# Kernel optimization log

Measured on AMD Instinct MI355X. Metric: run time of the kernel, lower is better.

## Reference

```python
import jax, jax.numpy as jnp
import numpy as np

N = 100000      # nodes
E = 1600000     # directed edges (before self-loops)
IN = 128        # in_channels
HID = 64        # hidden_channels
LH = 4          # local heads
GH = 2          # global heads
NC = 2          # num_classes
BN_EPS = 1e-5
NEG_SLOPE = 0.2


def setup_inputs() -> dict:
    key = jax.random.key(0)
    ks = jax.random.split(key, 24)
    def nrm(k, shape, fan_in):
        return jax.random.normal(k, shape, dtype=jnp.float32) / np.sqrt(fan_in)
    inp = {
        "x": jax.random.normal(ks[0], (N, IN), dtype=jnp.float32),
        "edge_index": jax.random.randint(ks[1], (2, E), 0, N, dtype=jnp.int64),
        # local GATConv: IN -> HID, heads=LH, concat
        "w1": nrm(ks[2], (IN, LH * HID), IN),
        "a_src1": nrm(ks[3], (LH, HID), HID),
        "a_dst1": nrm(ks[4], (LH, HID), HID),
        "b1": jnp.zeros((LH * HID,), jnp.float32),
        # BN1 over LH*HID
        "g1": jnp.ones((LH * HID,), jnp.float32),
        "be1": jnp.zeros((LH * HID,), jnp.float32),
        "m1": 0.1 * jax.random.normal(ks[5], (LH * HID,), dtype=jnp.float32),
        "v1": 0.5 + jax.random.uniform(ks[6], (LH * HID,), dtype=jnp.float32),
        # global GATConv: LH*HID -> HID, heads=GH, concat=False (mean)
        "w2": nrm(ks[7], (LH * HID, GH * HID), LH * HID),
        "a_src2": nrm(ks[8], (GH, HID), HID),
        "a_dst2": nrm(ks[9], (GH, HID), HID),
        "b2": jnp.zeros((HID,), jnp.float32),
        # BN2 over HID
        "g2": jnp.ones((HID,), jnp.float32),
        "be2": jnp.zeros((HID,), jnp.float32),
        "m2": 0.1 * jax.random.normal(ks[10], (HID,), dtype=jnp.float32),
        "v2": 0.5 + jax.random.uniform(ks[11], (HID,), dtype=jnp.float32),
        # classifier HID -> NC
        "wc": nrm(ks[12], (HID, NC), HID),
        "bc": jnp.zeros((NC,), jnp.float32),
    }
    return inp


def _gat_conv(x, src, dst, W, att_src, att_dst, bias, heads, out_c, concat):
    n = x.shape[0]
    h = (x @ W).reshape(n, heads, out_c)           # [N,H,C]
    a_s = jnp.sum(h * att_src, axis=-1)            # [N,H]
    a_d = jnp.sum(h * att_dst, axis=-1)            # [N,H]
    e = jax.nn.leaky_relu(a_s[src] + a_d[dst], NEG_SLOPE)  # [E,H]
    # segment softmax over destination node
    mx = jax.ops.segment_max(e, dst, num_segments=n)
    e = jnp.exp(e - mx[dst])
    den = jax.ops.segment_sum(e, dst, num_segments=n)
    alpha = e / (den[dst] + 1e-16)                 # [E,H]
    msg = h[src] * alpha[:, :, None]               # [E,H,C]
    out = jax.ops.segment_sum(msg, dst, num_segments=n)   # [N,H,C]
    out = out.reshape(n, heads * out_c) if concat else out.mean(axis=1)
    return out + bias


def _bn_eval(x, gamma, beta, mean, var):
    return (x - mean) * (gamma / jnp.sqrt(var + BN_EPS)) + beta


def reference(x, edge_index, w1, a_src1, a_dst1, b1, g1, be1, m1, v1,
              w2, a_src2, a_dst2, b2, g2, be2, m2, v2, wc, bc):
    n = x.shape[0]
    loops = jnp.arange(n, dtype=edge_index.dtype)
    src = jnp.concatenate([edge_index[0], loops])  # PyG adds self-loops
    dst = jnp.concatenate([edge_index[1], loops])
    # local attention layer
    h = _gat_conv(x, src, dst, w1, a_src1, a_dst1, b1, LH, HID, True)
    h = jax.nn.elu(_bn_eval(h, g1, be1, m1, v1))
    # global attention layer (last: mean over heads, no activation)
    h = _gat_conv(h, src, dst, w2, a_src2, a_dst2, b2, GH, HID, False)
    h = _bn_eval(h, g2, be2, m2, v2)
    return h @ wc + bc                             # [N, NC] logits
```

## Files before the change

kernel.cpp:

```cpp
#include <hip/hip_runtime.h>
#include <hip/hip_fp16.h>
#include <math.h>

#define NN 100000
#define EE 1600000
#define ETOT (EE + NN)
#define BN_EPS 1e-5f
#define NEG_SLOPE 0.2f
#define NBLK ((NN + 255) / 256)
#define GXM ((NN + 127) / 128)
#define NGRP 8
#define GRPSZ ((NN + NGRP - 1) / NGRP)

typedef _Float16 half8 __attribute__((ext_vector_type(8)));
typedef float f32x4 __attribute__((ext_vector_type(4)));

__device__ __forceinline__ float lrelu(float x) { return fmaxf(x, NEG_SLOPE * x); }
__device__ __forceinline__ float wsum(float v) {
#pragma unroll
    for (int m = 32; m; m >>= 1) v += __shfl_xor(v, m, 64);
    return v;
}
__device__ __forceinline__ float gsum16(float v) {
#pragma unroll
    for (int m = 1; m < 16; m <<= 1) v += __shfl_xor(v, m, 64);
    return v;
}
__device__ __forceinline__ unsigned packh2(float a, float b) {
    __half2 p = __float22half2_rn(make_float2(a, b));
    return *reinterpret_cast<unsigned*>(&p);
}

__global__ __launch_bounds__(256) void k_hist8(const int* __restrict__ ei,
                                               int* __restrict__ counts) {
    const int g = blockIdx.x & (NGRP - 1);
    const int lo = g * GRPSZ;
    const int hi = (lo + GRPSZ < NN) ? lo + GRPSZ : NN;
    const int nb = gridDim.x >> 3;
    const int stride = nb * 256;
    for (int e = (blockIdx.x >> 3) * 256 + threadIdx.x; e < EE; e += stride) {
        const int d = ei[EE + e];
        if (d >= lo && d < hi) atomicAdd(&counts[d], 1);
    }
}
__global__ __launch_bounds__(256) void k_scatter8(const int* __restrict__ ei,
                                                  int* __restrict__ srcs,
                                                  int* __restrict__ cursor) {
    const int g = blockIdx.x & (NGRP - 1);
    const int lo = g * GRPSZ;
    const int hi = (lo + GRPSZ < NN) ? lo + GRPSZ : NN;
    const int nb = gridDim.x >> 3;
    const int stride = nb * 256;
    for (int e = (blockIdx.x >> 3) * 256 + threadIdx.x; e < EE; e += stride) {
        const int d = ei[EE + e];
        if (d >= lo && d < hi) {
            const int p = atomicAdd(&cursor[d], 1);
            srcs[p] = ei[e];
        }
    }
}
__global__ __launch_bounds__(256) void k_scan_bsum(const int* __restrict__ counts,
                                                   int* __restrict__ bsum) {
    __shared__ int sd[256];
    const int i = blockIdx.x * 256 + threadIdx.x;
    sd[threadIdx.x] = (i < NN) ? counts[i] + 1 : 0;
    __syncthreads();
    for (int s2 = 128; s2; s2 >>= 1) {
        if (threadIdx.x < s2) sd[threadIdx.x] += sd[threadIdx.x + s2];
        __syncthreads();
    }
    if (threadIdx.x == 0) bsum[blockIdx.x] = sd[0];
}
__global__ __launch_bounds__(512) void k_scan_top(int* __restrict__ bsum, int nb) {
    __shared__ int sd[512];
    const int t = threadIdx.x;
    const int orig = (t < nb) ? bsum[t] : 0;
    sd[t] = orig;
    __syncthreads();
    for (int off = 1; off < 512; off <<= 1) {
        const int v = (t >= off) ? sd[t - off] : 0;
        __syncthreads();
        sd[t] += v;
        __syncthreads();
    }
    if (t < nb) bsum[t] = sd[t] - orig;
}
__global__ __launch_bounds__(256) void k_scan_final(const int* __restrict__ counts,
                                                    const int* __restrict__ bsum_ex,
                                                    int* __restrict__ rowptr,
                                                    int* __restrict__ srcs,
                                                    int* __restrict__ cursor) {
    __shared__ int sd[256];
    const int i = blockIdx.x * 256 + threadIdx.x;
    const int orig = (i < NN) ? counts[i] + 1 : 0;
    sd[threadIdx.x] = orig;
    __syncthreads();
    for (int off = 1; off < 256; off <<= 1) {
        const int v = (threadIdx.x >= off) ? sd[threadIdx.x - off] : 0;
        __syncthreads();
        sd[threadIdx.x] += v;
        __syncthreads();
    }
    if (i < NN) {
        const int rp = bsum_ex[blockIdx.x] + sd[threadIdx.x] - orig;
        rowptr[i] = rp;
        srcs[rp] = i;
        cursor[i] = rp + 1;
        if (i == NN - 1) rowptr[NN] = ETOT;
    }
}

__global__ __launch_bounds__(256) void k_prep(
    const float* __restrict__ b1, const float* __restrict__ g1,
    const float* __restrict__ be1, const float* __restrict__ m1,
    const float* __restrict__ v1,
    const float* __restrict__ b2, const float* __restrict__ g2,
    const float* __restrict__ be2, const float* __restrict__ m2,
    const float* __restrict__ v2, const float* __restrict__ wc,
    const float* __restrict__ bc,
    const float* __restrict__ w1, const float* __restrict__ w2,
    const float* __restrict__ as1w, const float* __restrict__ ad1w,
    float* __restrict__ scs, float* __restrict__ shs,
    float* __restrict__ wq, float* __restrict__ cst,
    float* __restrict__ va, float* __restrict__ vd,
    _Float16* __restrict__ wt1, _Float16* __restrict__ wt2,
    int* __restrict__ counts)
{
    const int b = blockIdx.x, t = threadIdx.x;
    if (b == 0) {
        const float sc = g1[t] * rsqrtf(v1[t] + BN_EPS);
        scs[t] = sc;
        shs[t] = (b1[t] - m1[t]) * sc + be1[t];
    } else if (b == 1) {
        if (t < 64) {
            const float s2 = g2[t] * rsqrtf(v2[t] + BN_EPS);
            wq[t * 2 + 0] = s2 * wc[t * 2 + 0];
            wq[t * 2 + 1] = s2 * wc[t * 2 + 1];
            const float tv = (b2[t] - m2[t]) * s2 + be2[t];
            const float c0 = wsum(tv * wc[t * 2 + 0]);
            const float c1 = wsum(tv * wc[t * 2 + 1]);
            if (t == 0) { cst[0] = c0 + bc[0]; cst[1] = c1 + bc[1]; }
        }
    } else if (b < 130) {
        const int idx = (b - 2) * 256 + t;
        const int n = idx >> 7, k = idx & 127;
        wt1[idx] = (_Float16)w1[k * 256 + n];
    } else if (b < 258) {
        const int idx = (b - 130) * 256 + t;
        const int n = idx >> 8, k = idx & 255;
        wt2[idx] = (_Float16)w2[k * 128 + n];
    } else if (b == 258) {
#pragma unroll
        for (int rep = 0; rep < 2; ++rep) {
            const int idx = rep * 256 + t;
            const int h = idx >> 7, k = idx & 127;
            float sa = 0.f, sd = 0.f;
            for (int c = 0; c < 64; ++c) {
                const float wv = w1[k * 256 + h * 64 + c];
                sa = fmaf(wv, as1w[h * 64 + c], sa);
                sd = fmaf(wv, ad1w[h * 64 + c], sd);
            }
            va[idx] = sa;
            vd[idx] = sd;
        }
    } else {
        const int i = (b - 259) * 256 + t;
        if (i < NN) counts[i] = 0;
    }
}

__global__ __launch_bounds__(256) void k_xcvt(
    const float* __restrict__ x, const float* __restrict__ va,
    const float* __restrict__ vd, _Float16* __restrict__ xh,
    float* __restrict__ as_, float* __restrict__ ad_)
{
    const int gid = blockIdx.x * 256 + threadIdx.x;
    const int n = gid >> 4;
    if (n >= NN) return;
    const int j = gid & 15;
    const int k0 = j * 8;
    float xv[8];
    *(float4*)&xv[0] = *(const float4*)&x[(size_t)n * 128 + k0];
    *(float4*)&xv[4] = *(const float4*)&x[(size_t)n * 128 + k0 + 4];
    half8 hv;
#pragma unroll
    for (int i = 0; i < 8; ++i) hv[i] = (_Float16)xv[i];
    *(half8*)&xh[(size_t)n * 128 + k0] = hv;
    float sa[4], sd[4];
#pragma unroll
    for (int h = 0; h < 4; ++h) {
        float s = 0.f, d = 0.f;
#pragma unroll
        for (int i = 0; i < 8; ++i) {
            s = fmaf(xv[i], va[h * 128 + k0 + i], s);
            d = fmaf(xv[i], vd[h * 128 + k0 + i], d);
        }
        sa[h] = gsum16(s);
        sd[h] = gsum16(d);
    }
    if (j == 0) {
        *(float4*)&as_[n * 4] = make_float4(sa[0], sa[1], sa[2], sa[3]);
        *(float4*)&ad_[n * 4] = make_float4(sd[0], sd[1], sd[2], sd[3]);
    }
}

__global__ __launch_bounds__(256) void k_agg1x(
    const int* __restrict__ rowptr, const int* __restrict__ srcs,
    const _Float16* __restrict__ xh, const float* __restrict__ as_,
    const float* __restrict__ ad_, _Float16* __restrict__ y)
{
    const int d = blockIdx.x * 4 + (threadIdx.x >> 6);
    if (d >= NN) return;
    const int lane = threadIdx.x & 63;
    const int r0 = rowptr[d], r1 = rowptr[d + 1];
    const int h = lane >> 4;
    const int cb = (lane & 15) * 8;
    const float myad = ad_[d * 4 + h];

    float den = 0.f;
    float acc[8] = {0.f, 0.f, 0.f, 0.f, 0.f, 0.f, 0.f, 0.f};
    int k = r0;
    for (; k + 3 < r1; k += 4) {
        const int s0 = srcs[k], s1 = srcs[k + 1], s2 = srcs[k + 2], s3 = srcs[k + 3];
        const float p0 = __expf(lrelu(as_[s0 * 4 + h] + myad));
        const float p1 = __expf(lrelu(as_[s1 * 4 + h] + myad));
        const float p2 = __expf(lrelu(as_[s2 * 4 + h] + myad));
        const float p3 = __expf(lrelu(as_[s3 * 4 + h] + myad));
        const half8 v0 = *(const half8*)&xh[(size_t)s0 * 128 + cb];
        const half8 v1 = *(const half8*)&xh[(size_t)s1 * 128 + cb];
        const half8 v2 = *(const half8*)&xh[(size_t)s2 * 128 + cb];
        const half8 v3 = *(const half8*)&xh[(size_t)s3 * 128 + cb];
        den += (p0 + p1) + (p2 + p3);
#pragma unroll
        for (int i = 0; i < 8; ++i) {
            acc[i] = fmaf(p0, (float)v0[i], acc[i]);
            acc[i] = fmaf(p1, (float)v1[i], acc[i]);
            acc[i] = fmaf(p2, (float)v2[i], acc[i]);
            acc[i] = fmaf(p3, (float)v3[i], acc[i]);
        }
    }
    for (; k < r1; ++k) {
        const int s = srcs[k];
        const float p = __expf(lrelu(as_[s * 4 + h] + myad));
        den += p;
        const half8 v = *(const half8*)&xh[(size_t)s * 128 + cb];
#pragma unroll
        for (int i = 0; i < 8; ++i) acc[i] = fmaf(p, (float)v[i], acc[i]);
    }
    const float inv = 1.f / (den + 1e-16f);
    half8 hv;
#pragma unroll
    for (int i = 0; i < 8; ++i) hv[i] = (_Float16)(acc[i] * inv);
    *(half8*)&y[(size_t)d * 512 + h * 128 + cb] = hv;
}

__global__ __launch_bounds__(256) void k_bd1(
    const _Float16* __restrict__ y, const _Float16* __restrict__ wt,
    const float* __restrict__ scs, const float* __restrict__ shs,
    _Float16* __restrict__ agg)
{
    __shared__ _Float16 ys[128][136];
    const int n0 = blockIdx.x * 128;
    const int t = threadIdx.x;
    const int l = t & 63, w = t >> 6;
    const int m0w = (w & 1) * 64, n0w = (w >> 1) * 32;
    const int lc = l & 15, kq = (l >> 4) * 8, lr = (l >> 4) * 4;

    for (int h = 0; h < 4; ++h) {
        if (h) __syncthreads();
#pragma unroll
        for (int i = 0; i < 8; ++i) {
            const int f = i * 2048 + t * 8;
            const int m = f >> 7, k8 = f & 127;
            half8 v = {};
            if (n0 + m < NN)
                v = *(const half8*)&y[(size_t)(n0 + m) * 512 + h * 128 + k8];
            *(half8*)&ys[m][k8] = v;
        }
        __syncthreads();

        const f32x4 fzero = {0.f, 0.f, 0.f, 0.f};
        f32x4 acc[4][2];
#pragma unroll
        for (int r = 0; r < 4; ++r) { acc[r][0] = fzero; acc[r][1] = fzero; }

#pragma unroll
        for (int ks = 0; ks < 4; ++ks) {
            const int k0 = ks * 32 + kq;
            const half8 a0 = *(const half8*)&ys[m0w + 0  + lc][k0];
            const half8 a1 = *(const half8*)&ys[m0w + 16 + lc][k0];
            const half8 a2 = *(const half8*)&ys[m0w + 32 + lc][k0];
            const half8 a3 = *(const half8*)&ys[m0w + 48 + lc][k0];
#pragma unroll
            for (int c = 0; c < 2; ++c) {
                const half8 b = *(const half8*)&wt[(size_t)(h * 64 + n0w + c * 16 + lc) * 128 + k0];
                acc[0][c] = __builtin_amdgcn_mfma_f32_16x16x32_f16(a0, b, acc[0][c], 0, 0, 0);
                acc[1][c] = __builtin_amdgcn_mfma_f32_16x16x32_f16(a1, b, acc[1][c], 0, 0, 0);
                acc[2][c] = __builtin_amdgcn_mfma_f32_16x16x32_f16(a2, b, acc[2][c], 0, 0, 0);
                acc[3][c] = __builtin_amdgcn_mfma_f32_16x16x32_f16(a3, b, acc[3][c], 0, 0, 0);
            }
        }

        const int j0 = h * 64 + n0w + lc;
        const float sc0 = scs[j0],      sh0 = shs[j0];
        const float sc1 = scs[j0 + 16], sh1 = shs[j0 + 16];
#pragma unroll
        for (int r = 0; r < 4; ++r) {
#pragma unroll
            for (int i = 0; i < 4; ++i) {
                const int rg = n0 + m0w + r * 16 + lr + i;
                if (rg < NN) {
                    float e0 = fmaf(acc[r][0][i], sc0, sh0);
                    float e1 = fmaf(acc[r][1][i], sc1, sh1);
                    e0 = e0 > 0.f ? e0 : __expf(e0) - 1.f;
                    e1 = e1 > 0.f ? e1 : __expf(e1) - 1.f;
                    _Float16* ap = agg + (size_t)rg * 256 + j0;
                    ap[0]  = (_Float16)e0;
                    ap[16] = (_Float16)e1;
                }
            }
        }
    }
}

__global__ __launch_bounds__(256) void k_gemm2m(
    const _Float16* __restrict__ agg, const _Float16* __restrict__ wt,
    const float* __restrict__ asrc, const float* __restrict__ adst,
    const float* __restrict__ wq,
    float* __restrict__ ad_, uint2* __restrict__ pack)
{
    __shared__ _Float16 xs[128][136];
    const int n0 = blockIdx.x * 128;
    const int t = threadIdx.x;
    const int l = t & 63, w = t >> 6;
    const int m0w = (w & 1) * 64, n0w = (w >> 1) * 64;
    const int lc = l & 15, kq = (l >> 4) * 8, lr = (l >> 4) * 4;

    const f32x4 fzero = {0.f, 0.f, 0.f, 0.f};
    f32x4 acc[4][4];
#pragma unroll
    for (int r = 0; r < 4; ++r)
#pragma unroll
        for (int c = 0; c < 4; ++c) acc[r][c] = fzero;

    const _Float16* abase = agg + (size_t)n0 * 256;
    for (int kc = 0; kc < 2; ++kc) {
        if (kc) __syncthreads();
#pragma unroll
        for (int i = 0; i < 8; ++i) {
            const int f = i * 2048 + t * 8;
            const int m = f >> 7, k8 = f & 127;
            half8 v = {};
            if (n0 + m < NN)
                v = *(const half8*)(abase + (size_t)m * 256 + kc * 128 + k8);
            *(half8*)&xs[m][k8] = v;
        }
        __syncthreads();

#pragma unroll
        for (int ks = 0; ks < 4; ++ks) {
            const int k0 = ks * 32 + kq;
            const int kgf = kc * 128 + k0;
            const half8 a0 = *(const half8*)&xs[m0w + 0  + lc][k0];
            const half8 a1 = *(const half8*)&xs[m0w + 16 + lc][k0];
            const half8 a2 = *(const half8*)&xs[m0w + 32 + lc][k0];
            const half8 a3 = *(const half8*)&xs[m0w + 48 + lc][k0];
#pragma unroll
            for (int c = 0; c < 4; ++c) {
                const half8 b = *(const half8*)&wt[(size_t)(n0w + c * 16 + lc) * 256 + kgf];
                acc[0][c] = __builtin_amdgcn_mfma_f32_16x16x32_f16(a0, b, acc[0][c], 0, 0, 0);
                acc[1][c] = __builtin_amdgcn_mfma_f32_16x16x32_f16(a1, b, acc[1][c], 0, 0, 0);
                acc[2][c] = __builtin_amdgcn_mfma_f32_16x16x32_f16(a2, b, acc[2][c], 0, 0, 0);
                acc[3][c] = __builtin_amdgcn_mfma_f32_16x16x32_f16(a3, b, acc[3][c], 0, 0, 0);
            }
        }
    }

    const int head = n0w >> 6;
    float awv[4], dwv[4], wq0[4], wq1[4];
#pragma unroll
    for (int c = 0; c < 4; ++c) {
        const int j = n0w + c * 16 + lc;
        const int cl = j & 63;
        awv[c] = asrc[j];
        dwv[c] = adst[j];
        wq0[c] = wq[cl * 2 + 0];
        wq1[c] = wq[cl * 2 + 1];
    }
#pragma unroll
    for (int r = 0; r < 4; ++r) {
#pragma unroll
        for (int i = 0; i < 4; ++i) {
            float s = 0.f, d = 0.f, q0 = 0.f, q1 = 0.f;
#pragma unroll
            for (int c = 0; c < 4; ++c) {
                s = fmaf(acc[r][c][i], awv[c], s);
                d = fmaf(acc[r][c][i], dwv[c], d);
                q0 = fmaf(acc[r][c][i], wq0[c], q0);
                q1 = fmaf(acc[r][c][i], wq1[c], q1);
            }
            s = gsum16(s); d = gsum16(d); q0 = gsum16(q0); q1 = gsum16(q1);
            const int rg = n0 + m0w + r * 16 + lr + i;
            if (lc == 0 && rg < NN) {
                ad_[rg * 2 + head] = d;
                uint2 u;
                u.x = __float_as_uint(s);
                u.y = packh2(q0, q1);
                pack[rg * 2 + head] = u;
            }
        }
    }
}

__global__ __launch_bounds__(256) void k_agg2q(
    const int* __restrict__ rowptr, const int* __restrict__ srcs,
    const uint4* __restrict__ pack, const float* __restrict__ ad_,
    const float* __restrict__ cst, float* __restrict__ out)
{
    const int d = blockIdx.x * 16 + (threadIdx.x >> 4);
    if (d >= NN) return;
    const int il = threadIdx.x & 15;
    const int r0 = rowptr[d], r1 = rowptr[d + 1];
    const float2 adv = *(const float2*)&ad_[d * 2];

    float den0 = 0.f, den1 = 0.f;
    float qa00 = 0.f, qa01 = 0.f, qa10 = 0.f, qa11 = 0.f;
    for (int k = r0 + il; k < r1; k += 16) {
        const int s = srcs[k];
        const uint4 rec = pack[s];
        const float a0 = __uint_as_float(rec.x);
        const float a1 = __uint_as_float(rec.z);
        const float2 q0 = __half22float2(*reinterpret_cast<const __half2*>(&rec.y));
        const float2 q1 = __half22float2(*reinterpret_cast<const __half2*>(&rec.w));
        const float p0 = __expf(lrelu(a0 + adv.x));
        const float p1 = __expf(lrelu(a1 + adv.y));
        den0 += p0; den1 += p1;
        qa00 = fmaf(p0, q0.x, qa00); qa01 = fmaf(p0, q0.y, qa01);
        qa10 = fmaf(p1, q1.x, qa10); qa11 = fmaf(p1, q1.y, qa11);
    }
    den0 = gsum16(den0); den1 = gsum16(den1);
    qa00 = gsum16(qa00); qa01 = gsum16(qa01);
    qa10 = gsum16(qa10); qa11 = gsum16(qa11);
    if (il == 0) {
        const float i0 = 1.f / (den0 + 1e-16f);
        const float i1 = 1.f / (den1 + 1e-16f);
        out[d * 2 + 0] = cst[0] + 0.5f * (qa00 * i0 + qa10 * i1);
        out[d * 2 + 1] = cst[1] + 0.5f * (qa01 * i0 + qa11 * i1);
    }
}

extern "C" void kernel_launch(void* const* d_in, const int* in_sizes, int n_in,
                              void* d_out, int out_size, void* d_ws, size_t ws_size,
                              hipStream_t stream) {
    const float* x      = (const float*)d_in[0];
    const int*   ei     = (const int*)d_in[1];
    const float* w1     = (const float*)d_in[2];
    const float* a_src1 = (const float*)d_in[3];
    const float* a_dst1 = (const float*)d_in[4];
    const float* b1     = (const float*)d_in[5];
    const float* g1     = (const float*)d_in[6];
    const float* be1    = (const float*)d_in[7];
    const float* m1     = (const float*)d_in[8];
    const float* v1     = (const float*)d_in[9];
    const float* w2     = (const float*)d_in[10];
    const float* a_src2 = (const float*)d_in[11];
    const float* a_dst2 = (const float*)d_in[12];
    const float* b2     = (const float*)d_in[13];
    const float* g2     = (const float*)d_in[14];
    const float* be2    = (const float*)d_in[15];
    const float* m2     = (const float*)d_in[16];
    const float* v2     = (const float*)d_in[17];
    const float* wc     = (const float*)d_in[18];
    const float* bc     = (const float*)d_in[19];
    float* out = (float*)d_out;

    float* ws = (float*)d_ws;
    _Float16* xh    = (_Float16*)ws;
    _Float16* y     = (_Float16*)(ws + (size_t)NN * 64);
    _Float16* agg1h = (_Float16*)(ws + (size_t)NN * 320);
    float* C = ws + (size_t)NN * 448;

    float* as1 = C;
    float* ad1 = C + (size_t)NN * 4;
    float* ad2 = C + (size_t)NN * 8;
    float* packf = C + (size_t)NN * 10;
    float* scs = C + (size_t)NN * 14;
    float* shs = scs + 256;
    float* wq  = shs + 256;
    float* cst = wq + 128;
    float* va  = cst + 64;
    float* vd  = va + 512;
    float* wbase = vd + 512;
    _Float16* wt1 = (_Float16*)wbase;
    _Float16* wt2 = wt1 + 32768;
    int* counts = (int*)(wbase + 32768);
    int* rowptr = counts + NN;
    int* bsum   = rowptr + NN + 63;
    int* srcs   = bsum + 512;

    k_prep<<<259 + NBLK, 256, 0, stream>>>(b1, g1, be1, m1, v1, b2, g2, be2, m2, v2,
                                           wc, bc, w1, w2, a_src1, a_dst1,
                                           scs, shs, wq, cst, va, vd, wt1, wt2, counts);
    k_hist8<<<2048, 256, 0, stream>>>(ei, counts);
    k_scan_bsum<<<NBLK, 256, 0, stream>>>(counts, bsum);
    k_scan_top<<<1, 512, 0, stream>>>(bsum, NBLK);
    k_scan_final<<<NBLK, 256, 0, stream>>>(counts, bsum, rowptr, srcs, counts);
    k_scatter8<<<2048, 256, 0, stream>>>(ei, srcs, counts);

    k_xcvt<<<(NN * 16 + 255) / 256, 256, 0, stream>>>(x, va, vd, xh, as1, ad1);
    k_agg1x<<<(NN + 3) / 4, 256, 0, stream>>>(rowptr, srcs, xh, as1, ad1, y);
    k_bd1<<<GXM, 256, 0, stream>>>(y, wt1, scs, shs, agg1h);

    k_gemm2m<<<GXM, 256, 0, stream>>>(agg1h, wt2, a_src2, a_dst2, wq,
                                      ad2, (uint2*)packf);
    k_agg2q<<<(NN + 15) / 16, 256, 0, stream>>>(rowptr, srcs, (const uint4*)packf,
                                                ad2, cst, out);
}
```

Measured before the change: 378.0 us.

## Fuse layer-1 GEMM with layer-2 GEMM, merge hist into prep, collapse scan kernels

Fuses the per-head layer-1 projection+BN+ELU GEMM with the layer-2 GEMM through a shared-memory intermediate, so the 256-wide fp16 activation never round-trips through global memory. The degree histogram is folded into the prep kernel, with counts zeroed by a memset. The top-level scan is merged into the final scan by having each block reduce the preceding block sums. The agg1 loop now loads srcs/attention scores once per lane and broadcasts them with shuffles. Tiles shrink to 64 rows with more shared memory per block, and the redundant block-sum reads in every scan block add some work.

New measurement: 360.2 us. -4.7%, faster.

```diff
diff --git a/kernel.cpp b/kernel.cpp
--- a/kernel.cpp
+++ b/kernel.cpp
@@ -8,9 +8,9 @@
 #define BN_EPS 1e-5f
 #define NEG_SLOPE 0.2f
 #define NBLK ((NN + 255) / 256)
-#define GXM ((NN + 127) / 128)
 #define NGRP 8
 #define GRPSZ ((NN + NGRP - 1) / NGRP)
+#define HISTBLK 2048
 
 typedef _Float16 half8 __attribute__((ext_vector_type(8)));
 typedef float f32x4 __attribute__((ext_vector_type(4)));
@@ -31,86 +31,7 @@
     return *reinterpret_cast<unsigned*>(&p);
 }
 
-__global__ __launch_bounds__(256) void k_hist8(const int* __restrict__ ei,
-                                               int* __restrict__ counts) {
-    const int g = blockIdx.x & (NGRP - 1);
-    const int lo = g * GRPSZ;
-    const int hi = (lo + GRPSZ < NN) ? lo + GRPSZ : NN;
-    const int nb = gridDim.x >> 3;
-    const int stride = nb * 256;
-    for (int e = (blockIdx.x >> 3) * 256 + threadIdx.x; e < EE; e += stride) {
-        const int d = ei[EE + e];
-        if (d >= lo && d < hi) atomicAdd(&counts[d], 1);
-    }
-}
-__global__ __launch_bounds__(256) void k_scatter8(const int* __restrict__ ei,
-                                                  int* __restrict__ srcs,
-                                                  int* __restrict__ cursor) {
-    const int g = blockIdx.x & (NGRP - 1);
-    const int lo = g * GRPSZ;
-    const int hi = (lo + GRPSZ < NN) ? lo + GRPSZ : NN;
-    const int nb = gridDim.x >> 3;
-    const int stride = nb * 256;
-    for (int e = (blockIdx.x >> 3) * 256 + threadIdx.x; e < EE; e += stride) {
-        const int d = ei[EE + e];
-        if (d >= lo && d < hi) {
-            const int p = atomicAdd(&cursor[d], 1);
-            srcs[p] = ei[e];
-        }
-    }
-}
-__global__ __launch_bounds__(256) void k_scan_bsum(const int* __restrict__ counts,
-                                                   int* __restrict__ bsum) {
-    __shared__ int sd[256];
-    const int i = blockIdx.x * 256 + threadIdx.x;
-    sd[threadIdx.x] = (i < NN) ? counts[i] + 1 : 0;
-    __syncthreads();
-    for (int s2 = 128; s2; s2 >>= 1) {
-        if (threadIdx.x < s2) sd[threadIdx.x] += sd[threadIdx.x + s2];
-        __syncthreads();
-    }
-    if (threadIdx.x == 0) bsum[blockIdx.x] = sd[0];
-}
-__global__ __launch_bounds__(512) void k_scan_top(int* __restrict__ bsum, int nb) {
-    __shared__ int sd[512];
-    const int t = threadIdx.x;
-    const int orig = (t < nb) ? bsum[t] : 0;
-    sd[t] = orig;
-    __syncthreads();
-    for (int off = 1; off < 512; off <<= 1) {
-        const int v = (t >= off) ? sd[t - off] : 0;
-        __syncthreads();
-        sd[t] += v;
-        __syncthreads();
-    }
-    if (t < nb) bsum[t] = sd[t] - orig;
-}
-__global__ __launch_bounds__(256) void k_scan_final(const int* __restrict__ counts,
-                                                    const int* __restrict__ bsum_ex,
-                                                    int* __restrict__ rowptr,
-                                                    int* __restrict__ srcs,
-                                                    int* __restrict__ cursor) {
-    __shared__ int sd[256];
-    const int i = blockIdx.x * 256 + threadIdx.x;
-    const int orig = (i < NN) ? counts[i] + 1 : 0;
-    sd[threadIdx.x] = orig;
-    __syncthreads();
-    for (int off = 1; off < 256; off <<= 1) {
-        const int v = (threadIdx.x >= off) ? sd[threadIdx.x - off] : 0;
-        __syncthreads();
-        sd[threadIdx.x] += v;
-        __syncthreads();
-    }
-    if (i < NN) {
-        const int rp = bsum_ex[blockIdx.x] + sd[threadIdx.x] - orig;
-        rowptr[i] = rp;
-        srcs[rp] = i;
-        cursor[i] = rp + 1;
-        if (i == NN - 1) rowptr[NN] = ETOT;
-    }
-}
-
-__global__ __launch_bounds__(256) void k_prep(
+__global__ __launch_bounds__(256) void k_preph(
     const float* __restrict__ b1, const float* __restrict__ g1,
     const float* __restrict__ be1, const float* __restrict__ m1,
     const float* __restrict__ v1,
@@ -120,6 +41,7 @@
     const float* __restrict__ bc,
     const float* __restrict__ w1, const float* __restrict__ w2,
     const float* __restrict__ as1w, const float* __restrict__ ad1w,
+    const int* __restrict__ ei,
     float* __restrict__ scs, float* __restrict__ shs,
     float* __restrict__ wq, float* __restrict__ cst,
     float* __restrict__ va, float* __restrict__ vd,
@@ -164,8 +86,78 @@
             vd[idx] = sd;
         }
     } else {
-        const int i = (b - 259) * 256 + t;
-        if (i < NN) counts[i] = 0;
+        const int bh = b - 259;
+        const int g = bh & (NGRP - 1);
+        const int lo = g * GRPSZ;
+        const int hi = (lo + GRPSZ < NN) ? lo + GRPSZ : NN;
+        const int stride = (HISTBLK >> 3) * 256;
+        for (int e = (bh >> 3) * 256 + t; e < EE; e += stride) {
+            const int d = ei[EE + e];
+            if (d >= lo && d < hi) atomicAdd(&counts[d], 1);
+        }
+    }
+}
+
+__global__ __launch_bounds__(256) void k_scan_bsum(const int* __restrict__ counts,
+                                                   int* __restrict__ bsum) {
+    __shared__ int sd[256];
+    const int i = blockIdx.x * 256 + threadIdx.x;
+    sd[threadIdx.x] = (i < NN) ? counts[i] + 1 : 0;
+    __syncthreads();
+    for (int s2 = 128; s2; s2 >>= 1) {
+        if (threadIdx.x < s2) sd[threadIdx.x] += sd[threadIdx.x + s2];
+        __syncthreads();
+    }
+    if (threadIdx.x == 0) bsum[blockIdx.x] = sd[0];
+}
+__global__ __launch_bounds__(256) void k_scan_finaltop(
+    const int* __restrict__ counts, const int* __restrict__ bsum,
+    int* __restrict__ rowptr, int* __restrict__ srcs, int* __restrict__ cursor)
+{
+    __shared__ int sd[256];
+    int partial = 0;
+    for (int j = threadIdx.x; j < NBLK; j += 256)
+        if (j < blockIdx.x) partial += bsum[j];
+    sd[threadIdx.x] = partial;
+    __syncthreads();
+    for (int s2 = 128; s2; s2 >>= 1) {
+        if (threadIdx.x < s2) sd[threadIdx.x] += sd[threadIdx.x + s2];
+        __syncthreads();
+    }
+    const int base = sd[0];
+    __syncthreads();
+    const int i = blockIdx.x * 256 + threadIdx.x;
+    const int orig = (i < NN) ? counts[i] + 1 : 0;
+    sd[threadIdx.x] = orig;
+    __syncthreads();
+    for (int off = 1; off < 256; off <<= 1) {
+        const int v = (threadIdx.x >= off) ? sd[threadIdx.x - off] : 0;
+        __syncthreads();
+        sd[threadIdx.x] += v;
+        __syncthreads();
+    }
+    if (i < NN) {
+        const int rp = base + sd[threadIdx.x] - orig;
+        rowptr[i] = rp;
+        srcs[rp] = i;
+        cursor[i] = rp + 1;
+        if (i == NN - 1) rowptr[NN] = ETOT;
+    }
+}
+__global__ __launch_bounds__(256) void k_scatter8(const int* __restrict__ ei,
+                                                  int* __restrict__ srcs,
+                                                  int* __restrict__ cursor) {
+    const int g = blockIdx.x & (NGRP - 1);
+    const int lo = g * GRPSZ;
+    const int hi = (lo + GRPSZ < NN) ? lo + GRPSZ : NN;
+    const int nb = gridDim.x >> 3;
+    const int stride = nb * 256;
+    for (int e = (blockIdx.x >> 3) * 256 + threadIdx.x; e < EE; e += stride) {
+        const int d = ei[EE + e];
+        if (d >= lo && d < hi) {
+            const int p = atomicAdd(&cursor[d], 1);
+            srcs[p] = ei[e];
+        }
     }
 }
 
@@ -221,16 +213,22 @@
     float acc[8] = {0.f, 0.f, 0.f, 0.f, 0.f, 0.f, 0.f, 0.f};
     int k = r0;
     for (; k + 3 < r1; k += 4) {
-        const int s0 = srcs[k], s1 = srcs[k + 1], s2 = srcs[k + 2], s3 = srcs[k + 3];
-        const float p0 = __expf(lrelu(as_[s0 * 4 + h] + myad));
-        const float p1 = __expf(lrelu(as_[s1 * 4 + h] + myad));
-        const float p2 = __expf(lrelu(as_[s2 * 4 + h] + myad));
-        const float p3 = __expf(lrelu(as_[s3 * 4 + h] + myad));
+        const int sm = srcs[k + (lane & 3)];
+        const float pm = __expf(lrelu(as_[sm * 4 + h] + myad));
+        const int s0 = __shfl(sm, 0, 64);
+        const int s1 = __shfl(sm, 1, 64);
+        const int s2 = __shfl(sm, 2, 64);
+        const int s3 = __shfl(sm, 3, 64);
+        const int pb = lane & 48;
+        const float p0 = __shfl(pm, pb | 0, 64);
+        const float p1 = __shfl(pm, pb | 1, 64);
+        const float p2 = __shfl(pm, pb | 2, 64);
+        const float p3 = __shfl(pm, pb | 3, 64);
+        den += (p0 + p1) + (p2 + p3);
         const half8 v0 = *(const half8*)&xh[(size_t)s0 * 128 + cb];
         const half8 v1 = *(const half8*)&xh[(size_t)s1 * 128 + cb];
         const half8 v2 = *(const half8*)&xh[(size_t)s2 * 128 + cb];
         const half8 v3 = *(const half8*)&xh[(size_t)s3 * 128 + cb];
-        den += (p0 + p1) + (p2 + p3);
 #pragma unroll
         for (int i = 0; i < 8; ++i) {
             acc[i] = fmaf(p0, (float)v0[i], acc[i]);
@@ -254,22 +252,29 @@
     *(half8*)&y[(size_t)d * 512 + h * 128 + cb] = hv;
 }
 
-__global__ __launch_bounds__(256) void k_bd1(
-    const _Float16* __restrict__ y, const _Float16* __restrict__ wt,
+__global__ __launch_bounds__(256) void k_l2fuse(
+    const _Float16* __restrict__ y,
+    const _Float16* __restrict__ wt1,
+    const _Float16* __restrict__ wt2,
     const float* __restrict__ scs, const float* __restrict__ shs,
-    _Float16* __restrict__ agg)
-{
-    __shared__ _Float16 ys[128][136];
-    const int n0 = blockIdx.x * 128;
+    const float* __restrict__ asrc, const float* __restrict__ adst,
+    const float* __restrict__ wq,
+    float* __restrict__ ad_, uint2* __restrict__ pack)
+{
+    __shared__ _Float16 ys[64][136];
+    __shared__ _Float16 mid[64][264];
+    const int n0 = blockIdx.x * 64;
     const int t = threadIdx.x;
     const int l = t & 63, w = t >> 6;
-    const int m0w = (w & 1) * 64, n0w = (w >> 1) * 32;
     const int lc = l & 15, kq = (l >> 4) * 8, lr = (l >> 4) * 4;
-
+    const int m0w = (w & 1) * 32;
+    const f32x4 fzero = {0.f, 0.f, 0.f, 0.f};
+
+    const int c0w = (w >> 1) * 32;
     for (int h = 0; h < 4; ++h) {
         if (h) __syncthreads();
 #pragma unroll
-        for (int i = 0; i < 8; ++i) {
+        for (int i = 0; i < 4; ++i) {
             const int f = i * 2048 + t * 8;
             const int m = f >> 7, k8 = f & 127;
             half8 v = {};
@@ -279,108 +284,60 @@
         }
         __syncthreads();
 
-        const f32x4 fzero = {0.f, 0.f, 0.f, 0.f};
-        f32x4 acc[4][2];
-#pragma unroll
-        for (int r = 0; r < 4; ++r) { acc[r][0] = fzero; acc[r][1] = fzero; }
-
+        f32x4 acc[2][2];
+        acc[0][0] = fzero; acc[0][1] = fzero; acc[1][0] = fzero; acc[1][1] = fzero;
 #pragma unroll
         for (int ks = 0; ks < 4; ++ks) {
             const int k0 = ks * 32 + kq;
-            const half8 a0 = *(const half8*)&ys[m0w + 0  + lc][k0];
+            const half8 a0 = *(const half8*)&ys[m0w + lc][k0];
             const half8 a1 = *(const half8*)&ys[m0w + 16 + lc][k0];
-            const half8 a2 = *(const half8*)&ys[m0w + 32 + lc][k0];
-            const half8 a3 = *(const half8*)&ys[m0w + 48 + lc][k0];
-#pragma unroll
-            for (int c = 0; c < 2; ++c) {
-                const half8 b = *(const half8*)&wt[(size_t)(h * 64 + n0w + c * 16 + lc) * 128 + k0];
-                acc[0][c] = __builtin_amdgcn_mfma_f32_16x16x32_f16(a0, b, acc[0][c], 0, 0, 0);
-                acc[1][c] = __builtin_amdgcn_mfma_f32_16x16x32_f16(a1, b, acc[1][c], 0, 0, 0);
-                acc[2][c] = __builtin_amdgcn_mfma_f32_16x16x32_f16(a2, b, acc[2][c], 0, 0, 0);
-                acc[3][c] = __builtin_amdgcn_mfma_f32_16x16x32_f16(a3, b, acc[3][c], 0, 0, 0);
-            }
-        }
-
-        const int j0 = h * 64 + n0w + lc;
-        const float sc0 = scs[j0],      sh0 = shs[j0];
-        const float sc1 = scs[j0 + 16], sh1 = shs[j0 + 16];
-#pragma unroll
-        for (int r = 0; r < 4; ++r) {
-#pragma unroll
-            for (int i = 0; i < 4; ++i) {
-                const int rg = n0 + m0w + r * 16 + lr + i;
-                if (rg < NN) {
-                    float e0 = fmaf(acc[r][0][i], sc0, sh0);
-                    float e1 = fmaf(acc[r][1][i], sc1, sh1);
-                    e0 = e0 > 0.f ? e0 : __expf(e0) - 1.f;
-                    e1 = e1 > 0.f ? e1 : __expf(e1) - 1.f;
-                    _Float16* ap = agg + (size_t)rg * 256 + j0;
-                    ap[0]  = (_Float16)e0;
-                    ap[16] = (_Float16)e1;
+            const half8 b0 = *(const half8*)&wt1[(size_t)(h * 64 + c0w + lc) * 128 + k0];
+            const half8 b1 = *(const half8*)&wt1[(size_t)(h * 64 + c0w + 16 + lc) * 128 + k0];
+            acc[0][0] = __builtin_amdgcn_mfma_f32_16x16x32_f16(a0, b0, acc[0][0], 0, 0, 0);
+            acc[0][1] = __builtin_amdgcn_mfma_f32_16x16x32_f16(a0, b1, acc[0][1], 0, 0, 0);
+            acc[1][0] = __builtin_amdgcn_mfma_f32_16x16x32_f16(a1, b0, acc[1][0], 0, 0, 0);
+            acc[1][1] = __builtin_amdgcn_mfma_f32_16x16x32_f16(a1, b1, acc[1][1], 0, 0, 0);
+        }
+#pragma unroll
+        for (int c = 0; c < 2; ++c) {
+            const int col = h * 64 + c0w + c * 16 + lc;
+            const float scv = scs[col], shv = shs[col];
+#pragma unroll
+            for (int r = 0; r < 2; ++r) {
+#pragma unroll
+                for (int i = 0; i < 4; ++i) {
+                    float e = fmaf(acc[r][c][i], scv, shv);
+                    e = e > 0.f ? e : __expf(e) - 1.f;
+                    mid[m0w + r * 16 + lr + i][col] = (_Float16)e;
                 }
             }
         }
     }
-}
-
-__global__ __launch_bounds__(256) void k_gemm2m(
-    const _Float16* __restrict__ agg, const _Float16* __restrict__ wt,
-    const float* __restrict__ asrc, const float* __restrict__ adst,
-    const float* __restrict__ wq,
-    float* __restrict__ ad_, uint2* __restrict__ pack)
-{
-    __shared__ _Float16 xs[128][136];
-    const int n0 = blockIdx.x * 128;
-    const int t = threadIdx.x;
-    const int l = t & 63, w = t >> 6;
-    const int m0w = (w & 1) * 64, n0w = (w >> 1) * 64;
-    const int lc = l & 15, kq = (l >> 4) * 8, lr = (l >> 4) * 4;
-
-    const f32x4 fzero = {0.f, 0.f, 0.f, 0.f};
-    f32x4 acc[4][4];
-#pragma unroll
-    for (int r = 0; r < 4; ++r)
-#pragma unroll
-        for (int c = 0; c < 4; ++c) acc[r][c] = fzero;
-
-    const _Float16* abase = agg + (size_t)n0 * 256;
-    for (int kc = 0; kc < 2; ++kc) {
-        if (kc) __syncthreads();
-#pragma unroll
-        for (int i = 0; i < 8; ++i) {
-            const int f = i * 2048 + t * 8;
-            const int m = f >> 7, k8 = f & 127;
-            half8 v = {};
-            if (n0 + m < NN)
-                v = *(const half8*)(abase + (size_t)m * 256 + kc * 128 + k8);
-            *(half8*)&xs[m][k8] = v;
-        }
-        __syncthreads();
-
-#pragma unroll
-        for (int ks = 0; ks < 4; ++ks) {
-            const int k0 = ks * 32 + kq;
-            const int kgf = kc * 128 + k0;
-            const half8 a0 = *(const half8*)&xs[m0w + 0  + lc][k0];
-            const half8 a1 = *(const half8*)&xs[m0w + 16 + lc][k0];
-            const half8 a2 = *(const half8*)&xs[m0w + 32 + lc][k0];
-            const half8 a3 = *(const half8*)&xs[m0w + 48 + lc][k0];
-#pragma unroll
-            for (int c = 0; c < 4; ++c) {
-                const half8 b = *(const half8*)&wt[(size_t)(n0w + c * 16 + lc) * 256 + kgf];
-                acc[0][c] = __builtin_amdgcn_mfma_f32_16x16x32_f16(a0, b, acc[0][c], 0, 0, 0);
-                acc[1][c] = __builtin_amdgcn_mfma_f32_16x16x32_f16(a1, b, acc[1][c], 0, 0, 0);
-                acc[2][c] = __builtin_amdgcn_mfma_f32_16x16x32_f16(a2, b, acc[2][c], 0, 0, 0);
-                acc[3][c] = __builtin_amdgcn_mfma_f32_16x16x32_f16(a3, b, acc[3][c], 0, 0, 0);
-            }
-        }
-    }
-
-    const int head = n0w >> 6;
+    __syncthreads();
+
+    const int c20 = (w >> 1) * 64;
+    f32x4 acc2[2][4];
+#pragma unroll
+    for (int r = 0; r < 2; ++r)
+#pragma unroll
+        for (int c = 0; c < 4; ++c) acc2[r][c] = fzero;
+#pragma unroll
+    for (int ks = 0; ks < 8; ++ks) {
+        const int k0 = ks * 32 + kq;
+        const half8 a0 = *(const half8*)&mid[m0w + lc][k0];
+        const half8 a1 = *(const half8*)&mid[m0w + 16 + lc][k0];
+#pragma unroll
+        for (int c = 0; c < 4; ++c) {
+            const half8 b = *(const half8*)&wt2[(size_t)(c20 + c * 16 + lc) * 256 + k0];
+            acc2[0][c] = __builtin_amdgcn_mfma_f32_16x16x32_f16(a0, b, acc2[0][c], 0, 0, 0);
+            acc2[1][c] = __builtin_amdgcn_mfma_f32_16x16x32_f16(a1, b, acc2[1][c], 0, 0, 0);
+        }
+    }
+    const int head = w >> 1;
     float awv[4], dwv[4], wq0[4], wq1[4];
 #pragma unroll
     for (int c = 0; c < 4; ++c) {
-        const int j = n0w + c * 16 + lc;
+        const int j = c20 + c * 16 + lc;
         const int cl = j & 63;
         awv[c] = asrc[j];
         dwv[c] = adst[j];
@@ -388,16 +345,16 @@
         wq1[c] = wq[cl * 2 + 1];
     }
 #pragma unroll
-    for (int r = 0; r < 4; ++r) {
+    for (int r = 0; r < 2; ++r) {
 #pragma unroll
         for (int i = 0; i < 4; ++i) {
             float s = 0.f, d = 0.f, q0 = 0.f, q1 = 0.f;
 #pragma unroll
             for (int c = 0; c < 4; ++c) {
-                s = fmaf(acc[r][c][i], awv[c], s);
-                d = fmaf(acc[r][c][i], dwv[c], d);
-                q0 = fmaf(acc[r][c][i], wq0[c], q0);
-                q1 = fmaf(acc[r][c][i], wq1[c], q1);
+                s = fmaf(acc2[r][c][i], awv[c], s);
+                d = fmaf(acc2[r][c][i], dwv[c], d);
+                q0 = fmaf(acc2[r][c][i], wq0[c], q0);
+                q1 = fmaf(acc2[r][c][i], wq1[c], q1);
             }
             s = gsum16(s); d = gsum16(d); q0 = gsum16(q0); q1 = gsum16(q1);
             const int rg = n0 + m0w + r * 16 + lr + i;
@@ -475,10 +432,9 @@
     float* out = (float*)d_out;
 
     float* ws = (float*)d_ws;
-    _Float16* xh    = (_Float16*)ws;
-    _Float16* y     = (_Float16*)(ws + (size_t)NN * 64);
-    _Float16* agg1h = (_Float16*)(ws + (size_t)NN * 320);
-    float* C = ws + (size_t)NN * 448;
+    _Float16* xh = (_Float16*)ws;
+    _Float16* y  = (_Float16*)(ws + (size_t)NN * 64);
+    float* C = ws + (size_t)NN * 320;
 
     float* as1 = C;
     float* ad1 = C + (size_t)NN * 4;
@@ -498,21 +454,22 @@
     int* bsum   = rowptr + NN + 63;
     int* srcs   = bsum + 512;
 
-    k_prep<<<259 + NBLK, 256, 0, stream>>>(b1, g1, be1, m1, v1, b2, g2, be2, m2, v2,
-                                           wc, bc, w1, w2, a_src1, a_dst1,
-                                           scs, shs, wq, cst, va, vd, wt1, wt2, counts);
-    k_hist8<<<2048, 256, 0, stream>>>(ei, counts);
+    hipMemsetAsync(counts, 0, (size_t)NN * sizeof(int), stream);
+    k_preph<<<259 + HISTBLK, 256, 0, stream>>>(
+        b1, g1, be1, m1, v1, b2, g2, be2, m2, v2, wc, bc, w1, w2,
+        a_src1, a_dst1, ei, scs, shs, wq, cst, va, vd, wt1, wt2, counts);
+
     k_scan_bsum<<<NBLK, 256, 0, stream>>>(counts, bsum);
-    k_scan_top<<<1, 512, 0, stream>>>(bsum, NBLK);
-    k_scan_final<<<NBLK, 256, 0, stream>>>(counts, bsum, rowptr, srcs, counts);
+    k_scan_finaltop<<<NBLK, 256, 0, stream>>>(counts, bsum, rowptr, srcs, counts);
     k_scatter8<<<2048, 256, 0, stream>>>(ei, srcs, counts);
 
     k_xcvt<<<(NN * 16 + 255) / 256, 256, 0, stream>>>(x, va, vd, xh, as1, ad1);
     k_agg1x<<<(NN + 3) / 4, 256, 0, stream>>>(rowptr, srcs, xh, as1, ad1, y);
-    k_bd1<<<GXM, 256, 0, stream>>>(y, wt1, scs, shs, agg1h);
-
-    k_gemm2m<<<GXM, 256, 0, stream>>>(agg1h, wt2, a_src2, a_dst2, wq,
-                                      ad2, (uint2*)packf);
+
+    k_l2fuse<<<(NN + 63) / 64, 256, 0, stream>>>(y, wt1, wt2, scs, shs,
+                                                 a_src2, a_dst2, wq,
+                                                 ad2, (uint2*)packf);
+
     k_agg2q<<<(NN + 15) / 16, 256, 0, stream>>>(rowptr, srcs, (const uint4*)packf,
                                                 ad2, cst, out);
 }
```
